# Performance work log

Hardware: AMD Instinct MI355X
Metric: run time of the kernel (lower is better)

The kernel has to match this reference:

```python
import jax, jax.numpy as jnp
import numpy as np
from jax import lax

RO = 4.0            # snake_config.ro (feature-map downsample ratio)
N_ADJ = 4           # snake_config.adj_num -> kernel = 2*4+1 = 9
K = 2 * N_ADJ + 1
DIL = (1, 1, 1, 2, 2, 4, 4)   # dilations of the 7 Snake residual circular convs
NMS_RADIUS = 2      # radius used in the iterative refinement cls_nms


def circ_conv(x, w, b, d):
    """Dilated circular conv along polygon axis. x:[N,C,P], w:[O,I,K]."""
    pad = N_ADJ * d
    xp = jnp.concatenate([x[..., -pad:], x, x[..., :pad]], axis=-1)
    y = lax.conv_general_dilated(xp, w, window_strides=(1,), padding='VALID',
                                 rhs_dilation=(d,),
                                 dimension_numbers=('NCH', 'OIH', 'NCH'))
    return y + b[None, :, None]


def conv1x1(x, w, b):
    # x:[N,C,P], w:[O,C] -> [N,O,P]
    return jnp.einsum('ncp,oc->nop', x, w) + b[None, :, None]


def bilinear_gather(cnn_feature, poly, ind):
    """grid_sample-style bilinear sampling (align_corners=False, zero pad).
    cnn_feature:[B,C,H,W], poly:[N,P,2] pixel coords, ind:[N] image index.
    Returns [N,C,P]."""
    B, C, H, W = cnn_feature.shape
    x = poly[..., 0] - 0.5
    y = poly[..., 1] - 0.5
    x0 = jnp.floor(x); y0 = jnp.floor(y)
    wx = x - x0; wy = y - y0
    x0i = x0.astype(jnp.int32); y0i = y0.astype(jnp.int32)

    def tap(yi, xi):
        valid = (xi >= 0) & (xi < W) & (yi >= 0) & (yi < H)
        xi_c = jnp.clip(xi, 0, W - 1)
        yi_c = jnp.clip(yi, 0, H - 1)
        f = cnn_feature[ind[:, None], :, yi_c, xi_c]  # [N,P,C]
        return f * valid[..., None]

    f00 = tap(y0i, x0i);     f01 = tap(y0i, x0i + 1)
    f10 = tap(y0i + 1, x0i); f11 = tap(y0i + 1, x0i + 1)
    out = (f00 * ((1 - wx) * (1 - wy))[..., None]
           + f01 * (wx * (1 - wy))[..., None]
           + f10 * ((1 - wx) * wy)[..., None]
           + f11 * (wx * wy)[..., None])
    return out.transpose(0, 2, 1)  # [N,C,P]


def cls_nms(cls, radius):
    """Circular local-max suppression of per-vertex scores. cls:[N,P,1]."""
    c = cls[..., 0]
    m = jnp.max(jnp.stack([jnp.roll(c, s, axis=1)
                           for s in range(-radius, radius + 1)], 0), axis=0)
    return jnp.where(c >= m, c, 0.0)[..., None]


def snake_body(x, head_w, head_b, res_w, res_b, fusion_w, fusion_b,
               pred1_w, pred1_b, pred2_w, pred2_b, pred3_w, pred3_b,
               cls1_w, cls1_b, cls2_w, cls2_b, cls3_w, cls3_b):
    h = jax.nn.relu(circ_conv(x, head_w, head_b, 1))
    states = [h]
    for i in range(7):  # fixed 7 residual layers, structurally distinct dilations
        r = jax.nn.relu(circ_conv(states[-1], res_w[i], res_b[i], DIL[i]))
        states.append(r + states[-1])
    state = jnp.concatenate(states, axis=1)                 # [N, 8*128, P]
    g = conv1x1(state, fusion_w, fusion_b)                  # [N, 256, P]
    g = jnp.max(g, axis=2, keepdims=True)
    g = jnp.broadcast_to(g, (state.shape[0], g.shape[1], state.shape[2]))
    state = jnp.concatenate([g, state], axis=1)             # [N, 1280, P]

    def head3(w1, b1, w2, b2, w3, b3):
        h1 = jax.nn.relu(conv1x1(state, w1, b1))
        h2 = jax.nn.relu(conv1x1(h1, w2, b2))
        return conv1x1(h2, w3, b3)

    offset = head3(pred1_w, pred1_b, pred2_w, pred2_b, pred3_w, pred3_b)  # [N,2,P]
    cls = head3(cls1_w, cls1_b, cls2_w, cls2_b, cls3_w, cls3_b)           # [N,1,P]
    return offset, cls


def setup_inputs() -> dict:
    key = jax.random.key(0)
    ks = jax.random.split(key, 32)
    B, C, H, W = 4, 64, 128, 128
    N, P = 512, 128
    SD = 128  # state_dim
    FD = 64 + 2 + 1  # feature_dim for iterative evolve_gcn
    std = 0.01  # conv init: normal(0, 0.01), bias 0 (matches module init)
    inp = {
        'cnn_feature': jax.random.normal(ks[0], (B, C, H, W), jnp.float32),
        'i_it_py': jax.random.uniform(ks[1], (N, P, 2), jnp.float32) * (W - 1),
        'c_it_py': jax.random.normal(ks[2], (N, P, 2), jnp.float32) * 0.2,
        'it_cls': jax.random.uniform(ks[3], (N, P), jnp.float32),
        'ind': jax.random.randint(ks[4], (N,), 0, B, jnp.int32),
        'head_w': jax.random.normal(ks[5], (SD, FD, K), jnp.float32) * std,
        'head_b': jnp.zeros((SD,), jnp.float32),
        'res_w': jax.random.normal(ks[6], (7, SD, SD, K), jnp.float32) * std,
        'res_b': jnp.zeros((7, SD), jnp.float32),
        'fusion_w': jax.random.normal(ks[7], (256, 8 * SD), jnp.float32) * std,
        'fusion_b': jnp.zeros((256,), jnp.float32),
        'pred1_w': jax.random.normal(ks[8], (256, 8 * SD + 256), jnp.float32) * std,
        'pred1_b': jnp.zeros((256,), jnp.float32),
        'pred2_w': jax.random.normal(ks[9], (64, 256), jnp.float32) * std,
        'pred2_b': jnp.zeros((64,), jnp.float32),
        'pred3_w': jax.random.normal(ks[10], (2, 64), jnp.float32) * std,
        'pred3_b': jnp.zeros((2,), jnp.float32),
        'cls1_w': jax.random.normal(ks[11], (256, 8 * SD + 256), jnp.float32) * std,
        'cls1_b': jnp.zeros((256,), jnp.float32),
        'cls2_w': jax.random.normal(ks[12], (64, 256), jnp.float32) * std,
        'cls2_b': jnp.zeros((64,), jnp.float32),
        'cls3_w': jax.random.normal(ks[13], (1, 64), jnp.float32) * std,
        'cls3_b': jnp.zeros((1,), jnp.float32),
    }
    return inp


def reference(cnn_feature, i_it_py, c_it_py, it_cls, ind,
              head_w, head_b, res_w, res_b, fusion_w, fusion_b,
              pred1_w, pred1_b, pred2_w, pred2_b, pred3_w, pred3_b,
              cls1_w, cls1_b, cls2_w, cls2_b, cls3_w, cls3_b):
    # evolve_poly: gather CNN features at vertices, concat scaled canonical
    # coords + per-vertex cls, run Snake, add offsets, NMS sigmoid scores.
    feat = bilinear_gather(cnn_feature, i_it_py, ind)        # [N,64,P]
    c = (c_it_py * RO).transpose(0, 2, 1)                    # [N,2,P]
    x = jnp.concatenate([feat, c, it_cls[:, None, :]], axis=1)  # [N,67,P]
    offset, cls = snake_body(x, head_w, head_b, res_w, res_b, fusion_w, fusion_b,
                             pred1_w, pred1_b, pred2_w, pred2_b, pred3_w, pred3_b,
                             cls1_w, cls1_b, cls2_w, cls2_b, cls3_w, cls3_b)
    i_poly = i_it_py * RO + offset.transpose(0, 2, 1)        # [N,P,2]
    cls = cls.transpose(0, 2, 1)                             # [N,P,1]
    nms = cls_nms(jax.nn.sigmoid(cls), NMS_RADIUS)           # [N,P,1]
    return i_poly, cls, nms
```

## Files before the change

### kernel.cpp

```cpp
#include <hip/hip_runtime.h>
#include <math.h>

typedef __attribute__((ext_vector_type(8))) short bf16x8;
typedef __attribute__((ext_vector_type(4))) float f32x4;

#define UOFF_CAW 0L
#define UOFF_FAW 2359296L
#define UOFF_H1W 2883584L
#define UOFF_W2F 3932160L
#define NB_TOT   3997696L
#define OFF_W1G  1998848L
#define OFF_DYN  2129920L
#define REPACK_N 4128768L

__device__ inline ushort f2bf_rne(float x) {
  uint u = __float_as_uint(x);
  return (ushort)((u + 0x7FFFu + ((u >> 16) & 1u)) >> 16);
}
__device__ inline void split_bf(float x, ushort& h, ushort& l) {
  uint u = __float_as_uint(x);
  uint hb = (u + 0x7FFFu + ((u >> 16) & 1u)) & 0xFFFF0000u;
  h = (ushort)(hb >> 16);
  l = f2bf_rne(x - __uint_as_float(hb));
}
__device__ inline ushort bfsel(float w, int split) {
  uint u = __float_as_uint(w);
  uint hb = (u + 0x7FFFu + ((u >> 16) & 1u)) & 0xFFFF0000u;
  if (split == 0) return (ushort)(hb >> 16);
  float lo = w - __uint_as_float(hb);
  uint ul = __float_as_uint(lo);
  return (ushort)((ul + 0x7FFFu + ((ul >> 16) & 1u)) >> 16);
}
__device__ inline bf16x8 asb(uint4 a) {
  union { uint4 u; bf16x8 v; } x; x.u = a; return x.v;
}
__device__ inline f32x4 MFMA_(bf16x8 a, bf16x8 b, f32x4 c) {
  return __builtin_amdgcn_mfma_f32_16x16x32_bf16(a, b, c, 0, 0, 0);
}
__device__ inline void bar_lgkm() {
  asm volatile("s_waitcnt lgkmcnt(0)" ::: "memory");
  __builtin_amdgcn_s_barrier();
}

__device__ inline void read_frag_pair(const char* xb, int pc, int g, int ic,
                                      bf16x8& bh, bf16x8& bl) {
  const int s0 = (pc & 7) << 4;
  const char* a = xb + pc * 512 + (((ic * 64 + (g << 4))) ^ s0);
  bh = asb(*(const uint4*)a);
  bl = asb(*(const uint4*)(a + 256));
}

__global__ void k_repack(const float* __restrict__ head_w, const float* __restrict__ res_w,
                         const float* __restrict__ fusion_w,
                         const float* __restrict__ pred1_w, const float* __restrict__ cls1_w,
                         const float* __restrict__ pred2_w, const float* __restrict__ cls2_w,
                         float* __restrict__ ws) {
  const long j = (long)blockIdx.x * 256 + threadIdx.x;
  if (j >= REPACK_N) return;
  if (j < NB_TOT) {
    ushort* wsu = (ushort*)ws;
    float w;
    if (j < UOFF_FAW) {
      int e = (int)(j & 7); long q = j >> 3;
      int lane = (int)(q & 63); q >>= 6;
      int mt = (int)(q & 1); q >>= 1;
      int split = (int)(q & 1); q >>= 1;
      int ic = (int)(q & 3); q >>= 2;
      int tap = (int)(q % 9); q /= 9;
      int mp = (int)(q & 3); int l = (int)(q >> 2);
      int gg = lane >> 4;
      int kl = (e < 4) ? (4 * gg + e) : (16 + 4 * gg + e - 4);
      int m = mp * 32 + mt * 16 + (lane & 15);
      int i = ic * 32 + kl;
      if (l == 0) w = (i < 67) ? head_w[((long)m * 67 + i) * 9 + tap] : 0.f;
      else        w = res_w[(((long)(l - 1) * 128 + m) * 128 + i) * 9 + tap];
      wsu[j] = bfsel(w, split);
    } else if (j < UOFF_H1W) {
      long jj = j - UOFF_FAW;
      int e = (int)(jj & 7); long q = jj >> 3;
      int lane = (int)(q & 63); q >>= 6;
      int mt = (int)(q & 1); q >>= 1;
      int split = (int)(q & 1); q >>= 1;
      int ic = (int)(q & 3); q >>= 2;
      int fm2 = (int)(q & 7); int l = (int)(q >> 3);
      int gg = lane >> 4;
      int kl = (e < 4) ? (4 * gg + e) : (16 + 4 * gg + e - 4);
      int m = fm2 * 32 + mt * 16 + (lane & 15);
      int i = ic * 32 + kl;
      w = fusion_w[(long)m * 1024 + l * 128 + i];
      wsu[j] = bfsel(w, split);
    } else if (j < UOFF_W2F) {
      long jj = j - UOFF_H1W;
      int e = (int)(jj & 7); long q = jj >> 3;
      int lane = (int)(q & 63); q >>= 6;
      int mt = (int)(q & 1); q >>= 1;
      int split = (int)(q & 1); q >>= 1;
      int ic = (int)(q & 3); q >>= 2;
      int slab = (int)(q & 7); q >>= 3;
      int mp = (int)(q & 7); int blk = (int)(q >> 3);
      int gg = lane >> 4;
      int kl = (e < 4) ? (4 * gg + e) : (16 + 4 * gg + e - 4);
      int m = blk * 256 + mp * 32 + mt * 16 + (lane & 15);
      int k = slab * 128 + ic * 32 + kl;
      w = (m < 256) ? pred1_w[(long)m * 1280 + 256 + k] : cls1_w[(long)(m - 256) * 1280 + 256 + k];
      wsu[j] = bfsel(w, split);
    } else {
      long jj = j - UOFF_W2F;
      int e = (int)(jj & 7); long q = jj >> 3;
      int lane = (int)(q & 63); q >>= 6;
      int split = (int)(q & 1); q >>= 1;
      int ic = (int)(q & 7); q >>= 3;
      int mfr = (int)(q & 3); int blk = (int)(q >> 2);
      int gg = lane >> 4;
      int kl = (e < 4) ? (4 * gg + e) : (16 + 4 * gg + e - 4);
      int m = mfr * 16 + (lane & 15);
      int k = ic * 32 + kl;
      w = blk ? cls2_w[(long)m * 256 + k] : pred2_w[(long)m * 256 + k];
      wsu[j] = bfsel(w, split);
    }
  } else {
    long q = j - NB_TOT; int o = (int)(q & 511); int c = (int)(q >> 9);
    ws[OFF_W1G + q] = (o < 256) ? pred1_w[(long)o * 1280 + c] : cls1_w[(long)(o - 256) * 1280 + c];
  }
}

__global__ __launch_bounds__(1024) __attribute__((amdgpu_waves_per_eu(4)))
void k_fused(const float* __restrict__ cnn, const float* __restrict__ i_it,
             const float* __restrict__ c_it, const float* __restrict__ cls_in,
             const int* __restrict__ ind,
             const ushort* __restrict__ CAW, const ushort* __restrict__ FAW,
             const ushort* __restrict__ H1W, const ushort* __restrict__ W2F,
             const float* __restrict__ head_b, const float* __restrict__ res_b,
             const float* __restrict__ fus_b, const float* __restrict__ W1G,
             const float* __restrict__ p1b, const float* __restrict__ c1b,
             const float* __restrict__ p2b, const float* __restrict__ c2b,
             const float* __restrict__ p3w, const float* __restrict__ p3b,
             const float* __restrict__ c3w, const float* __restrict__ c3b,
             float* __restrict__ states, float* __restrict__ out, int p0) {
  __shared__ uint4 xt4[4096];
  __shared__ float scr[512];
  __shared__ float sg[256];
  __shared__ float hg_s[512];
  char* xb = (char*)xt4;
  const int ln = blockIdx.x, n = p0 + ln, t = threadIdx.x;
  const int lane = t & 63, li = lane & 15, g = lane >> 4;
  const int wv = __builtin_amdgcn_readfirstlane(t >> 6);
  const int mp = wv & 3, np = wv >> 2;
  const int fm2 = wv & 7, fq = wv >> 3;
  const int mw = wv & 7, qw = wv >> 3;

  {
    const int p = t & 127, qg = t >> 7;
    const long nb = (long)n * 128 + p;
    const int sw = p & 7;
    if (qg < 4) {
      const float gx = i_it[nb * 2 + 0] - 0.5f;
      const float gy = i_it[nb * 2 + 1] - 0.5f;
      const float fx = floorf(gx), fy = floorf(gy);
      const float wx = gx - fx, wy = gy - fy;
      const int x0 = (int)fx, y0 = (int)fy, x1 = x0 + 1, y1 = y0 + 1;
      const bool vx0 = (x0 >= 0) & (x0 < 128), vx1 = (x1 >= 0) & (x1 < 128);
      const bool vy0 = (y0 >= 0) & (y0 < 128), vy1 = (y1 >= 0) & (y1 < 128);
      const int x0c = min(max(x0, 0), 127), x1c = min(max(x1, 0), 127);
      const int y0c = min(max(y0, 0), 127), y1c = min(max(y1, 0), 127);
      const float w00 = (vx0 && vy0) ? (1.f - wx) * (1.f - wy) : 0.f;
      const float w01 = (vx1 && vy0) ? wx * (1.f - wy) : 0.f;
      const float w10 = (vx0 && vy1) ? (1.f - wx) * wy : 0.f;
      const float w11 = (vx1 && vy1) ? wx * wy : 0.f;
      const long base = (long)ind[n] * (64L * 16384);
      const int a00 = y0c * 128 + x0c, a01 = y0c * 128 + x1c;
      const int a10 = y1c * 128 + x0c, a11 = y1c * 128 + x1c;
#pragma unroll
      for (int qq = 0; qq < 4; qq++) {
        ushort hh[4], ll[4];
#pragma unroll
        for (int cc = 0; cc < 4; cc++) {
          const int c = qg * 16 + qq * 4 + cc;
          const float* f = cnn + base + (long)c * 16384;
          float x = f[a00] * w00 + f[a01] * w01 + f[a10] * w10 + f[a11] * w11;
          split_bf(x, hh[cc], ll[cc]);
        }
        const int G = ((qg >> 1) * 4 + qq) ^ sw;
        char* a = xb + p * 512 + G * 16 + (qg & 1) * 8;
        *(uint2*)a = make_uint2((uint)hh[0] | ((uint)hh[1] << 16), (uint)hh[2] | ((uint)hh[3] << 16));
        *(uint2*)(a + 256) = make_uint2((uint)ll[0] | ((uint)ll[1] << 16), (uint)ll[2] | ((uint)ll[3] << 16));
      }
    } else {
#pragma unroll
      for (int qq = 0; qq < 4; qq++) {
        ushort hh[4], ll[4];
        if (qg == 4 && qq == 0) {
          float v0 = c_it[nb * 2 + 0] * 4.f, v1 = c_it[nb * 2 + 1] * 4.f, v2 = cls_in[nb];
          split_bf(v0, hh[0], ll[0]); split_bf(v1, hh[1], ll[1]); split_bf(v2, hh[2], ll[2]);
          hh[3] = 0; ll[3] = 0;
        } else {
          hh[0] = hh[1] = hh[2] = hh[3] = 0; ll[0] = ll[1] = ll[2] = ll[3] = 0;
        }
        const int G = ((qg >> 1) * 4 + qq) ^ sw;
        char* a = xb + p * 512 + G * 16 + (qg & 1) * 8;
        *(uint2*)a = make_uint2((uint)hh[0] | ((uint)hh[1] << 16), (uint)hh[2] | ((uint)hh[3] << 16));
        *(uint2*)(a + 256) = make_uint2((uint)ll[0] | ((uint)ll[1] << 16), (uint)ll[2] | ((uint)ll[3] << 16));
      }
    }
  }
  __syncthreads();

  const f32x4 fz = {0.f, 0.f, 0.f, 0.f};
  f32x4 facc[2][4];
#pragma unroll
  for (int a = 0; a < 2; a++)
#pragma unroll
    for (int b = 0; b < 4; b++) facc[a][b] = fz;

  const uint4* caw = (const uint4*)CAW;
  const uint4* faw = (const uint4*)FAW;
  uint4* stq = (uint4*)(states + (long)ln * 114688);

  for (int l = 0; l < 8; l++) {
    const int dil = (l >= 6) ? 4 : ((l >= 4) ? 2 : 1);
    const int nic = (l == 0) ? 3 : 4;
    if (l > 0) {
      uint4* dst = stq + (long)(l - 1) * 4096;
#pragma unroll
      for (int k = 0; k < 4; k++) dst[k * 1024 + t] = xt4[k * 1024 + t];
      const uint4* fawl = faw + ((long)((l - 1) * 8 + fm2)) * 1024 + lane;
#pragma unroll
      for (int ic = 0; ic < 4; ic++) {
        const uint4* w0 = fawl + ic * 256;
        const bf16x8 Ah0 = asb(w0[0]),   Ah1 = asb(w0[64]);
        const bf16x8 Al0 = asb(w0[128]), Al1 = asb(w0[192]);
#pragma unroll
        for (int nt = 0; nt < 4; nt++) {
          const int pc = fq * 64 + nt * 16 + li;
          bf16x8 bh, bl;
          read_frag_pair(xb, pc, g, ic, bh, bl);
          facc[0][nt] = MFMA_(Ah0, bh, facc[0][nt]);
          facc[1][nt] = MFMA_(Ah1, bh, facc[1][nt]);
          facc[0][nt] = MFMA_(Ah0, bl, facc[0][nt]);
          facc[1][nt] = MFMA_(Ah1, bl, facc[1][nt]);
          facc[0][nt] = MFMA_(Al0, bh, facc[0][nt]);
          facc[1][nt] = MFMA_(Al1, bh, facc[1][nt]);
        }
      }
    }
    f32x4 cacc[2][2];
    cacc[0][0] = fz; cacc[0][1] = fz; cacc[1][0] = fz; cacc[1][1] = fz;
    const uint4* cawl = caw + ((long)(l * 4 + mp)) * 9216;
    for (int tap = 0; tap < 9; tap++) {
      const int shift = (tap - 4) * dil;
      const int pc0 = (np * 32 + li + shift + 128) & 127;
      const int pc1 = (np * 32 + 16 + li + shift + 128) & 127;
      const uint4* cawt = cawl + tap * 1024 + lane;
      for (int ic = 0; ic < nic; ic++) {
        bf16x8 bh0, bl0, bh1, bl1;
        read_frag_pair(xb, pc0, g, ic, bh0, bl0);
        read_frag_pair(xb, pc1, g, ic, bh1, bl1);
        const uint4* w0 = cawt + ic * 256;
        const bf16x8 Ah0 = asb(w0[0]),   Ah1 = asb(w0[64]);
        const bf16x8 Al0 = asb(w0[128]), Al1 = asb(w0[192]);
        cacc[0][0] = MFMA_(Ah0, bh0, cacc[0][0]);
        cacc[0][1] = MFMA_(Ah0, bh1, cacc[0][1]);
        cacc[1][0] = MFMA_(Ah1, bh0, cacc[1][0]);
        cacc[1][1] = MFMA_(Ah1, bh1, cacc[1][1]);
        cacc[0][0] = MFMA_(Ah0, bl0, cacc[0][0]);
        cacc[0][1] = MFMA_(Ah0, bl1, cacc[0][1]);
        cacc[1][0] = MFMA_(Ah1, bl0, cacc[1][0]);
        cacc[1][1] = MFMA_(Ah1, bl1, cacc[1][1]);
        cacc[0][0] = MFMA_(Al0, bh0, cacc[0][0]);
        cacc[0][1] = MFMA_(Al0, bh1, cacc[0][1]);
        cacc[1][0] = MFMA_(Al1, bh0, cacc[1][0]);
        cacc[1][1] = MFMA_(Al1, bh1, cacc[1][1]);
      }
    }
    bar_lgkm();
    {
      const float* bsrc = (l == 0) ? head_b : (res_b + (l - 1) * 128);
      const float4 b0 = *(const float4*)&bsrc[mp * 32 + g * 4];
      const float4 b1 = *(const float4*)&bsrc[mp * 32 + 16 + g * 4];
#pragma unroll
      for (int nt = 0; nt < 2; nt++) {
        const int p = np * 32 + nt * 16 + li;
        const int X = (mp * 64 + g * 16) ^ ((p & 7) << 4);
        char* a = xb + p * 512 + X;
        float v[8];
        v[0] = fmaxf(cacc[0][nt][0] + b0.x, 0.f);
        v[1] = fmaxf(cacc[0][nt][1] + b0.y, 0.f);
        v[2] = fmaxf(cacc[0][nt][2] + b0.z, 0.f);
        v[3] = fmaxf(cacc[0][nt][3] + b0.w, 0.f);
        v[4] = fmaxf(cacc[1][nt][0] + b1.x, 0.f);
        v[5] = fmaxf(cacc[1][nt][1] + b1.y, 0.f);
        v[6] = fmaxf(cacc[1][nt][2] + b1.z, 0.f);
        v[7] = fmaxf(cacc[1][nt][3] + b1.w, 0.f);
        if (l > 0) {
          const uint4 oh = *(const uint4*)a;
          const uint4 ol = *(const uint4*)(a + 256);
          const uint hw[4] = {oh.x, oh.y, oh.z, oh.w};
          const uint lw[4] = {ol.x, ol.y, ol.z, ol.w};
#pragma unroll
          for (int k = 0; k < 8; k++) {
            const uint hh = (k & 1) ? (hw[k >> 1] & 0xFFFF0000u) : ((hw[k >> 1] & 0xFFFFu) << 16);
            const uint ll = (k & 1) ? (lw[k >> 1] & 0xFFFF0000u) : ((lw[k >> 1] & 0xFFFFu) << 16);
            v[k] += __uint_as_float(hh) + __uint_as_float(ll);
          }
        }
        ushort hh[8], ll[8];
#pragma unroll
        for (int k = 0; k < 8; k++) split_bf(v[k], hh[k], ll[k]);
        *(uint4*)a = make_uint4((uint)hh[0] | ((uint)hh[1] << 16), (uint)hh[2] | ((uint)hh[3] << 16),
                                (uint)hh[4] | ((uint)hh[5] << 16), (uint)hh[6] | ((uint)hh[7] << 16));
        *(uint4*)(a + 256) = make_uint4((uint)ll[0] | ((uint)ll[1] << 16), (uint)ll[2] | ((uint)ll[3] << 16),
                                        (uint)ll[4] | ((uint)ll[5] << 16), (uint)ll[6] | ((uint)ll[7] << 16));
      }
    }
    __syncthreads();
  }

  {
    const uint4* fawl = faw + ((long)(7 * 8 + fm2)) * 1024 + lane;
#pragma unroll
    for (int ic = 0; ic < 4; ic++) {
      const uint4* w0 = fawl + ic * 256;
      const bf16x8 Ah0 = asb(w0[0]),   Ah1 = asb(w0[64]);
      const bf16x8 Al0 = asb(w0[128]), Al1 = asb(w0[192]);
#pragma unroll
      for (int nt = 0; nt < 4; nt++) {
        const int pc = fq * 64 + nt * 16 + li;
        bf16x8 bh, bl;
        read_frag_pair(xb, pc, g, ic, bh, bl);
        facc[0][nt] = MFMA_(Ah0, bh, facc[0][nt]);
        facc[1][nt] = MFMA_(Ah1, bh, facc[1][nt]);
        facc[0][nt] = MFMA_(Ah0, bl, facc[0][nt]);
        facc[1][nt] = MFMA_(Ah1, bl, facc[1][nt]);
        facc[0][nt] = MFMA_(Al0, bh, facc[0][nt]);
        facc[1][nt] = MFMA_(Al1, bh, facc[1][nt]);
      }
    }
  }

#pragma unroll
  for (int mt = 0; mt < 2; mt++) {
#pragma unroll
    for (int r = 0; r < 4; r++) {
      float m = fmaxf(fmaxf(facc[mt][0][r], facc[mt][1][r]),
                      fmaxf(facc[mt][2][r], facc[mt][3][r]));
#pragma unroll
      for (int s = 1; s < 16; s <<= 1) m = fmaxf(m, __shfl_xor(m, s, 64));
      if (li == 0) scr[(fm2 * 32 + mt * 16 + g * 4 + r) * 2 + fq] = m;
    }
  }
  asm volatile("s_waitcnt vmcnt(0)" ::: "memory");
  bar_lgkm();
  if (t < 256) sg[t] = fmaxf(scr[2 * t], scr[2 * t + 1]) + fus_b[t];

  const uint4* sp = (const uint4*)stq;
  uint4 stg[4];
#pragma unroll
  for (int k = 0; k < 4; k++) stg[k] = sp[k * 1024 + t];
  bar_lgkm();

  if (t < 512) {
    float s = (t < 256) ? p1b[t] : c1b[t - 256];
    const float* w = W1G + t;
#pragma unroll 8
    for (int c = 0; c < 256; c++) s = fmaf(w[(long)c * 512], sg[c], s);
    hg_s[t] = s;
  }

  const uint4* aw = (const uint4*)H1W;
  f32x4 hacc[4][4];
#pragma unroll
  for (int f = 0; f < 4; f++)
#pragma unroll
    for (int c = 0; c < 4; c++) hacc[f][c] = fz;

#pragma unroll
  for (int ic = 0; ic < 4; ic++) {
    const uint4* w00 = aw + ((long)((2 * mw + 0) * 8 + 7)) * 1024 + ic * 256 + lane;
    const uint4* w01 = aw + ((long)((2 * mw + 1) * 8 + 7)) * 1024 + ic * 256 + lane;
    const bf16x8 Ah0 = asb(w00[0]),   Ah1 = asb(w00[64]);
    const bf16x8 Al0 = asb(w00[128]), Al1 = asb(w00[192]);
    const bf16x8 Ah2 = asb(w01[0]),   Ah3 = asb(w01[64]);
    const bf16x8 Al2 = asb(w01[128]), Al3 = asb(w01[192]);
#pragma unroll
    for (int nt = 0; nt < 4; nt++) {
      const int pc = qw * 64 + nt * 16 + li;
      bf16x8 bh, bl;
      read_frag_pair(xb, pc, g, ic, bh, bl);
      hacc[0][nt] = MFMA_(Ah0, bh, hacc[0][nt]);
      hacc[1][nt] = MFMA_(Ah1, bh, hacc[1][nt]);
      hacc[2][nt] = MFMA_(Ah2, bh, hacc[2][nt]);
      hacc[3][nt] = MFMA_(Ah3, bh, hacc[3][nt]);
      hacc[0][nt] = MFMA_(Ah0, bl, hacc[0][nt]);
      hacc[1][nt] = MFMA_(Ah1, bl, hacc[1][nt]);
      hacc[2][nt] = MFMA_(Ah2, bl, hacc[2][nt]);
      hacc[3][nt] = MFMA_(Ah3, bl, hacc[3][nt]);
      hacc[0][nt] = MFMA_(Al0, bh, hacc[0][nt]);
      hacc[1][nt] = MFMA_(Al1, bh, hacc[1][nt]);
      hacc[2][nt] = MFMA_(Al2, bh, hacc[2][nt]);
      hacc[3][nt] = MFMA_(Al3, bh, hacc[3][nt]);
    }
  }
  for (int s = 0; s < 7; s++) {
    bar_lgkm();
#pragma unroll
    for (int k = 0; k < 4; k++) xt4[k * 1024 + t] = stg[k];
    bar_lgkm();
    if (s < 6) {
#pragma unroll
      for (int k = 0; k < 4; k++) stg[k] = sp[(long)(s + 1) * 4096 + k * 1024 + t];
    }
#pragma unroll
    for (int ic = 0; ic < 4; ic++) {
      const uint4* w00 = aw + ((long)((2 * mw + 0) * 8 + s)) * 1024 + ic * 256 + lane;
      const uint4* w01 = aw + ((long)((2 * mw + 1) * 8 + s)) * 1024 + ic * 256 + lane;
      const bf16x8 Ah0 = asb(w00[0]),   Ah1 = asb(w00[64]);
      const bf16x8 Al0 = asb(w00[128]), Al1 = asb(w00[192]);
      const bf16x8 Ah2 = asb(w01[0]),   Ah3 = asb(w01[64]);
      const bf16x8 Al2 = asb(w01[128]), Al3 = asb(w01[192]);
#pragma unroll
      for (int nt = 0; nt < 4; nt++) {
        const int pc = qw * 64 + nt * 16 + li;
        bf16x8 bh, bl;
        read_frag_pair(xb, pc, g, ic, bh, bl);
        hacc[0][nt] = MFMA_(Ah0, bh, hacc[0][nt]);
        hacc[1][nt] = MFMA_(Ah1, bh, hacc[1][nt]);
        hacc[2][nt] = MFMA_(Ah2, bh, hacc[2][nt]);
        hacc[3][nt] = MFMA_(Ah3, bh, hacc[3][nt]);
        hacc[0][nt] = MFMA_(Ah0, bl, hacc[0][nt]);
        hacc[1][nt] = MFMA_(Ah1, bl, hacc[1][nt]);
        hacc[2][nt] = MFMA_(Ah2, bl, hacc[2][nt]);
        hacc[3][nt] = MFMA_(Ah3, bl, hacc[3][nt]);
        hacc[0][nt] = MFMA_(Al0, bh, hacc[0][nt]);
        hacc[1][nt] = MFMA_(Al1, bh, hacc[1][nt]);
        hacc[2][nt] = MFMA_(Al2, bh, hacc[2][nt]);
        hacc[3][nt] = MFMA_(Al3, bh, hacc[3][nt]);
      }
    }
  }
  bar_lgkm();

#pragma unroll
  for (int f = 0; f < 4; f++) {
    const float4 hq = *(const float4*)&hg_s[mw * 64 + f * 16 + g * 4];
#pragma unroll
    for (int nt = 0; nt < 4; nt++) {
      hacc[f][nt][0] = fmaxf(hacc[f][nt][0] + hq.x, 0.f);
      hacc[f][nt][1] = fmaxf(hacc[f][nt][1] + hq.y, 0.f);
      hacc[f][nt][2] = fmaxf(hacc[f][nt][2] + hq.z, 0.f);
      hacc[f][nt][3] = fmaxf(hacc[f][nt][3] + hq.w, 0.f);
    }
  }

  const uint4* w2 = (const uint4*)W2F;
  f32x4 a2q[4];
  for (int q = 0; q < 4; q++) {
    a2q[q] = fz;
    if (qw == (q >> 1)) {
#pragma unroll
      for (int fp = 0; fp < 4; fp += 2) {
        const int kc = 2 * mw + (fp >> 1);
#pragma unroll
        for (int ntl = 0; ntl < 2; ntl++) {
          const int nt = 2 * (q & 1) + ntl;
          const int pl = ntl * 16 + li;
          char* a = xb + pl * 2048 + ((kc * 64 + g * 16) ^ ((pl & 7) << 4));
          ushort hh[8], ll[8];
#pragma unroll
          for (int e = 0; e < 4; e++) { split_bf(hacc[fp][nt][e], hh[e], ll[e]); }
#pragma unroll
          for (int e = 0; e < 4; e++) { split_bf(hacc[fp + 1][nt][e], hh[4 + e], ll[4 + e]); }
          *(uint4*)a = make_uint4((uint)hh[0] | ((uint)hh[1] << 16), (uint)hh[2] | ((uint)hh[3] << 16),
                                  (uint)hh[4] | ((uint)hh[5] << 16), (uint)hh[6] | ((uint)hh[7] << 16));
          *(uint4*)(a + 1024) = make_uint4((uint)ll[0] | ((uint)ll[1] << 16), (uint)ll[2] | ((uint)ll[3] << 16),
                                           (uint)ll[4] | ((uint)ll[5] << 16), (uint)ll[6] | ((uint)ll[7] << 16));
        }
      }
    }
    bar_lgkm();
    {
      const int blkc = mw >> 2;
      const int pl = qw * 16 + li;
#pragma unroll
      for (int ic8 = 0; ic8 < 8; ic8++) {
        const int kc = blkc * 8 + ic8;
        const uint4* wb = w2 + (((long)(blkc * 4 + (mw & 3)) * 8 + ic8) * 2) * 64 + lane;
        const bf16x8 Ah = asb(wb[0]), Al = asb(wb[64]);
        const char* ba = xb + pl * 2048 + ((kc * 64 + g * 16) ^ ((pl & 7) << 4));
        const bf16x8 bh = asb(*(const uint4*)ba);
        const bf16x8 bl = asb(*(const uint4*)(ba + 1024));
        a2q[q] = MFMA_(Ah, bh, a2q[q]);
        a2q[q] = MFMA_(Ah, bl, a2q[q]);
        a2q[q] = MFMA_(Al, bh, a2q[q]);
      }
    }
    bar_lgkm();
  }

  {
    float* h2L = (float*)xb;
#pragma unroll
    for (int q = 0; q < 4; q++) {
#pragma unroll
      for (int e = 0; e < 4; e++) {
        const int row = mw * 16 + g * 4 + e;
        const float bb = (mw < 4) ? p2b[row] : c2b[row - 64];
        h2L[row * 128 + q * 32 + qw * 16 + li] = fmaxf(a2q[q][e] + bb, 0.f);
      }
    }
  }
  bar_lgkm();

  {
    const float* h2L = (const float*)xb;
    float sig = 0.f;
    const int pp = t & 127;
    if (t < 128) {
      float o0v = p3b[0], o1v = p3b[1], cv = c3b[0];
      for (int j = 0; j < 64; j++) {
        const float hp = h2L[j * 128 + pp];
        const float hc = h2L[(64 + j) * 128 + pp];
        o0v = fmaf(p3w[j], hp, o0v);
        o1v = fmaf(p3w[64 + j], hp, o1v);
        cv = fmaf(c3w[j], hc, cv);
      }
      const long ip = ((long)n * 128 + pp) * 2;
      out[ip + 0] = i_it[ip + 0] * 4.f + o0v;
      out[ip + 1] = i_it[ip + 1] * 4.f + o1v;
      out[131072 + (long)n * 128 + pp] = cv;
      sig = 1.f / (1.f + expf(-cv));
      scr[pp] = sig;
    }
    bar_lgkm();
    if (t < 128) {
      float m = scr[pp];
#pragma unroll
      for (int s = 1; s <= 2; s++) {
        m = fmaxf(m, scr[(pp + s) & 127]);
        m = fmaxf(m, scr[(pp + 128 - s) & 127]);
      }
      out[196608 + (long)n * 128 + pp] = (sig >= m) ? sig : 0.f;
    }
  }
}

extern "C" void kernel_launch(void* const* d_in, const int* in_sizes, int n_in,
                              void* d_out, int out_size, void* d_ws, size_t ws_size,
                              hipStream_t stream) {
  const float* cnn      = (const float*)d_in[0];
  const float* i_it     = (const float*)d_in[1];
  const float* c_it     = (const float*)d_in[2];
  const float* it_cls   = (const float*)d_in[3];
  const int*   ind      = (const int*)d_in[4];
  const float* head_w   = (const float*)d_in[5];
  const float* head_b   = (const float*)d_in[6];
  const float* res_w    = (const float*)d_in[7];
  const float* res_b    = (const float*)d_in[8];
  const float* fusion_w = (const float*)d_in[9];
  const float* fusion_b = (const float*)d_in[10];
  const float* pred1_w  = (const float*)d_in[11];
  const float* pred1_b  = (const float*)d_in[12];
  const float* pred2_w  = (const float*)d_in[13];
  const float* pred2_b  = (const float*)d_in[14];
  const float* pred3_w  = (const float*)d_in[15];
  const float* pred3_b  = (const float*)d_in[16];
  const float* cls1_w   = (const float*)d_in[17];
  const float* cls1_b   = (const float*)d_in[18];
  const float* cls2_w   = (const float*)d_in[19];
  const float* cls2_b   = (const float*)d_in[20];
  const float* cls3_w   = (const float*)d_in[21];
  const float* cls3_b   = (const float*)d_in[22];
  float* ws = (float*)d_ws;
  float* out = (float*)d_out;
  const ushort* wsu = (const ushort*)d_ws;

  k_repack<<<(int)((REPACK_N + 255) / 256), 256, 0, stream>>>(
      head_w, res_w, fusion_w, pred1_w, cls1_w, pred2_w, cls2_w, ws);

  long avail_f = (long)(ws_size / 4) - OFF_DYN;
  long Cl = avail_f / 114688;
  int C = (Cl >= 512) ? 512 : ((Cl >= 256) ? 256 : (int)(Cl < 1 ? 1 : Cl));
  float* states = ws + OFF_DYN;

  for (int p0 = 0; p0 < 512; p0 += C) {
    int Cc = (512 - p0 < C) ? (512 - p0) : C;
    k_fused<<<Cc, 1024, 0, stream>>>(cnn, i_it, c_it, it_cls, ind,
                                     wsu + UOFF_CAW, wsu + UOFF_FAW,
                                     wsu + UOFF_H1W, wsu + UOFF_W2F,
                                     head_b, res_b, fusion_b, ws + OFF_W1G,
                                     pred1_b, cls1_b, pred2_b, cls2_b,
                                     pred3_w, pred3_b, cls3_w, cls3_b,
                                     states, out, p0);
  }
}
```

Baseline: 1.033 ms.

## Fuse fusion and pred1/cls1 projections into per-layer accumulation, drop state spill

Concatenates the fusion conv weights and the state part of pred1/cls1 into one 768-row weight matrix, so each layer's state is multiplied into all three accumulations right after it is produced. This removes the global-memory spill and reload of the eight 128x128 layer states and the second pass over them. It also removes the chunked multi-launch loop in favour of a single launch. The cost is 24 accumulator tiles per wave instead of 8, which raises register pressure and may cut occupancy. The circular-conv inner loop is also reordered to load one B fragment pair at a time.

Measured after the change: 1.368 ms. +32.4%, slower.

```diff
diff --git a/kernel.cpp b/kernel.cpp
--- a/kernel.cpp
+++ b/kernel.cpp
@@ -5,12 +5,10 @@
 typedef __attribute__((ext_vector_type(4))) float f32x4;
 
 #define UOFF_CAW 0L
-#define UOFF_FAW 2359296L
-#define UOFF_H1W 2883584L
+#define UOFF_GW  2359296L
 #define UOFF_W2F 3932160L
 #define NB_TOT   3997696L
 #define OFF_W1G  1998848L
-#define OFF_DYN  2129920L
 #define REPACK_N 4128768L
 
 __device__ inline ushort f2bf_rne(float x) {
@@ -60,7 +58,7 @@
   if (j < NB_TOT) {
     ushort* wsu = (ushort*)ws;
     float w;
-    if (j < UOFF_FAW) {
+    if (j < UOFF_GW) {
       int e = (int)(j & 7); long q = j >> 3;
       int lane = (int)(q & 63); q >>= 6;
       int mt = (int)(q & 1); q >>= 1;
@@ -75,34 +73,21 @@
       if (l == 0) w = (i < 67) ? head_w[((long)m * 67 + i) * 9 + tap] : 0.f;
       else        w = res_w[(((long)(l - 1) * 128 + m) * 128 + i) * 9 + tap];
       wsu[j] = bfsel(w, split);
-    } else if (j < UOFF_H1W) {
-      long jj = j - UOFF_FAW;
+    } else if (j < UOFF_W2F) {
+      long jj = j - UOFF_GW;
       int e = (int)(jj & 7); long q = jj >> 3;
       int lane = (int)(q & 63); q >>= 6;
-      int mt = (int)(q & 1); q >>= 1;
       int split = (int)(q & 1); q >>= 1;
       int ic = (int)(q & 3); q >>= 2;
-      int fm2 = (int)(q & 7); int l = (int)(q >> 3);
+      int f = (int)(q % 3); q /= 3;
+      int wv = (int)(q & 15); int l = (int)(q >> 4);
       int gg = lane >> 4;
       int kl = (e < 4) ? (4 * gg + e) : (16 + 4 * gg + e - 4);
-      int m = fm2 * 32 + mt * 16 + (lane & 15);
-      int i = ic * 32 + kl;
-      w = fusion_w[(long)m * 1024 + l * 128 + i];
-      wsu[j] = bfsel(w, split);
-    } else if (j < UOFF_W2F) {
-      long jj = j - UOFF_H1W;
-      int e = (int)(jj & 7); long q = jj >> 3;
-      int lane = (int)(q & 63); q >>= 6;
-      int mt = (int)(q & 1); q >>= 1;
-      int split = (int)(q & 1); q >>= 1;
-      int ic = (int)(q & 3); q >>= 2;
-      int slab = (int)(q & 7); q >>= 3;
-      int mp = (int)(q & 7); int blk = (int)(q >> 3);
-      int gg = lane >> 4;
-      int kl = (e < 4) ? (4 * gg + e) : (16 + 4 * gg + e - 4);
-      int m = blk * 256 + mp * 32 + mt * 16 + (lane & 15);
-      int k = slab * 128 + ic * 32 + kl;
-      w = (m < 256) ? pred1_w[(long)m * 1280 + 256 + k] : cls1_w[(long)(m - 256) * 1280 + 256 + k];
+      int grow = wv * 48 + f * 16 + (lane & 15);
+      int k = ic * 32 + kl;
+      if (grow < 256)      w = fusion_w[(long)grow * 1024 + l * 128 + k];
+      else if (grow < 512) w = pred1_w[(long)(grow - 256) * 1280 + 256 + l * 128 + k];
+      else                 w = cls1_w[(long)(grow - 512) * 1280 + 256 + l * 128 + k];
       wsu[j] = bfsel(w, split);
     } else {
       long jj = j - UOFF_W2F;
@@ -128,25 +113,24 @@
 void k_fused(const float* __restrict__ cnn, const float* __restrict__ i_it,
              const float* __restrict__ c_it, const float* __restrict__ cls_in,
              const int* __restrict__ ind,
-             const ushort* __restrict__ CAW, const ushort* __restrict__ FAW,
-             const ushort* __restrict__ H1W, const ushort* __restrict__ W2F,
+             const ushort* __restrict__ CAW, const ushort* __restrict__ GW,
+             const ushort* __restrict__ W2F,
              const float* __restrict__ head_b, const float* __restrict__ res_b,
              const float* __restrict__ fus_b, const float* __restrict__ W1G,
              const float* __restrict__ p1b, const float* __restrict__ c1b,
              const float* __restrict__ p2b, const float* __restrict__ c2b,
              const float* __restrict__ p3w, const float* __restrict__ p3b,
              const float* __restrict__ c3w, const float* __restrict__ c3b,
-             float* __restrict__ states, float* __restrict__ out, int p0) {
+             float* __restrict__ out) {
   __shared__ uint4 xt4[4096];
-  __shared__ float scr[512];
+  __shared__ float scr[256];
   __shared__ float sg[256];
   __shared__ float hg_s[512];
   char* xb = (char*)xt4;
-  const int ln = blockIdx.x, n = p0 + ln, t = threadIdx.x;
+  const int n = blockIdx.x, t = threadIdx.x;
   const int lane = t & 63, li = lane & 15, g = lane >> 4;
   const int wv = __builtin_amdgcn_readfirstlane(t >> 6);
   const int mp = wv & 3, np = wv >> 2;
-  const int fm2 = wv & 7, fq = wv >> 3;
   const int mw = wv & 7, qw = wv >> 3;
 
   {
@@ -206,40 +190,42 @@
   __syncthreads();
 
   const f32x4 fz = {0.f, 0.f, 0.f, 0.f};
-  f32x4 facc[2][4];
-#pragma unroll
-  for (int a = 0; a < 2; a++)
-#pragma unroll
-    for (int b = 0; b < 4; b++) facc[a][b] = fz;
+  f32x4 acc[3][8];
+#pragma unroll
+  for (int f = 0; f < 3; f++)
+#pragma unroll
+    for (int c = 0; c < 8; c++) acc[f][c] = fz;
 
   const uint4* caw = (const uint4*)CAW;
-  const uint4* faw = (const uint4*)FAW;
-  uint4* stq = (uint4*)(states + (long)ln * 114688);
+  const uint4* gaw = (const uint4*)GW;
 
   for (int l = 0; l < 8; l++) {
     const int dil = (l >= 6) ? 4 : ((l >= 4) ? 2 : 1);
     const int nic = (l == 0) ? 3 : 4;
     if (l > 0) {
-      uint4* dst = stq + (long)(l - 1) * 4096;
-#pragma unroll
-      for (int k = 0; k < 4; k++) dst[k * 1024 + t] = xt4[k * 1024 + t];
-      const uint4* fawl = faw + ((long)((l - 1) * 8 + fm2)) * 1024 + lane;
+      const uint4* gwl = gaw + ((long)((l - 1) * 16 + wv)) * 1536 + lane;
 #pragma unroll
       for (int ic = 0; ic < 4; ic++) {
-        const uint4* w0 = fawl + ic * 256;
-        const bf16x8 Ah0 = asb(w0[0]),   Ah1 = asb(w0[64]);
-        const bf16x8 Al0 = asb(w0[128]), Al1 = asb(w0[192]);
-#pragma unroll
-        for (int nt = 0; nt < 4; nt++) {
-          const int pc = fq * 64 + nt * 16 + li;
+        const uint4* w0 = gwl + (0 * 4 + ic) * 128;
+        const uint4* w1 = gwl + (1 * 4 + ic) * 128;
+        const uint4* w2p = gwl + (2 * 4 + ic) * 128;
+        const bf16x8 Ah0 = asb(w0[0]), Al0 = asb(w0[64]);
+        const bf16x8 Ah1 = asb(w1[0]), Al1 = asb(w1[64]);
+        const bf16x8 Ah2 = asb(w2p[0]), Al2 = asb(w2p[64]);
+#pragma unroll
+        for (int nt = 0; nt < 8; nt++) {
+          const int pc = nt * 16 + li;
           bf16x8 bh, bl;
           read_frag_pair(xb, pc, g, ic, bh, bl);
-          facc[0][nt] = MFMA_(Ah0, bh, facc[0][nt]);
-          facc[1][nt] = MFMA_(Ah1, bh, facc[1][nt]);
-          facc[0][nt] = MFMA_(Ah0, bl, facc[0][nt]);
-          facc[1][nt] = MFMA_(Ah1, bl, facc[1][nt]);
-          facc[0][nt] = MFMA_(Al0, bh, facc[0][nt]);
-          facc[1][nt] = MFMA_(Al1, bh, facc[1][nt]);
+          acc[0][nt] = MFMA_(Ah0, bh, acc[0][nt]);
+          acc[1][nt] = MFMA_(Ah1, bh, acc[1][nt]);
+          acc[2][nt] = MFMA_(Ah2, bh, acc[2][nt]);
+          acc[0][nt] = MFMA_(Ah0, bl, acc[0][nt]);
+          acc[1][nt] = MFMA_(Ah1, bl, acc[1][nt]);
+          acc[2][nt] = MFMA_(Ah2, bl, acc[2][nt]);
+          acc[0][nt] = MFMA_(Al0, bh, acc[0][nt]);
+          acc[1][nt] = MFMA_(Al1, bh, acc[1][nt]);
+          acc[2][nt] = MFMA_(Al2, bh, acc[2][nt]);
         }
       }
     }
@@ -252,24 +238,24 @@
       const int pc1 = (np * 32 + 16 + li + shift + 128) & 127;
       const uint4* cawt = cawl + tap * 1024 + lane;
       for (int ic = 0; ic < nic; ic++) {
-        bf16x8 bh0, bl0, bh1, bl1;
-        read_frag_pair(xb, pc0, g, ic, bh0, bl0);
-        read_frag_pair(xb, pc1, g, ic, bh1, bl1);
         const uint4* w0 = cawt + ic * 256;
         const bf16x8 Ah0 = asb(w0[0]),   Ah1 = asb(w0[64]);
         const bf16x8 Al0 = asb(w0[128]), Al1 = asb(w0[192]);
-        cacc[0][0] = MFMA_(Ah0, bh0, cacc[0][0]);
-        cacc[0][1] = MFMA_(Ah0, bh1, cacc[0][1]);
-        cacc[1][0] = MFMA_(Ah1, bh0, cacc[1][0]);
-        cacc[1][1] = MFMA_(Ah1, bh1, cacc[1][1]);
-        cacc[0][0] = MFMA_(Ah0, bl0, cacc[0][0]);
-        cacc[0][1] = MFMA_(Ah0, bl1, cacc[0][1]);
-        cacc[1][0] = MFMA_(Ah1, bl0, cacc[1][0]);
-        cacc[1][1] = MFMA_(Ah1, bl1, cacc[1][1]);
-        cacc[0][0] = MFMA_(Al0, bh0, cacc[0][0]);
-        cacc[0][1] = MFMA_(Al0, bh1, cacc[0][1]);
-        cacc[1][0] = MFMA_(Al1, bh0, cacc[1][0]);
-        cacc[1][1] = MFMA_(Al1, bh1, cacc[1][1]);
+        bf16x8 bh, bl;
+        read_frag_pair(xb, pc0, g, ic, bh, bl);
+        cacc[0][0] = MFMA_(Ah0, bh, cacc[0][0]);
+        cacc[1][0] = MFMA_(Ah1, bh, cacc[1][0]);
+        cacc[0][0] = MFMA_(Ah0, bl, cacc[0][0]);
+        cacc[1][0] = MFMA_(Ah1, bl, cacc[1][0]);
+        cacc[0][0] = MFMA_(Al0, bh, cacc[0][0]);
+        cacc[1][0] = MFMA_(Al1, bh, cacc[1][0]);
+        read_frag_pair(xb, pc1, g, ic, bh, bl);
+        cacc[0][1] = MFMA_(Ah0, bh, cacc[0][1]);
+        cacc[1][1] = MFMA_(Ah1, bh, cacc[1][1]);
+        cacc[0][1] = MFMA_(Ah0, bl, cacc[0][1]);
+        cacc[1][1] = MFMA_(Ah1, bl, cacc[1][1]);
+        cacc[0][1] = MFMA_(Al0, bh, cacc[0][1]);
+        cacc[1][1] = MFMA_(Al1, bh, cacc[1][1]);
       }
     }
     bar_lgkm();
@@ -316,46 +302,50 @@
   }
 
   {
-    const uint4* fawl = faw + ((long)(7 * 8 + fm2)) * 1024 + lane;
+    const uint4* gwl = gaw + ((long)(7 * 16 + wv)) * 1536 + lane;
 #pragma unroll
     for (int ic = 0; ic < 4; ic++) {
-      const uint4* w0 = fawl + ic * 256;
-      const bf16x8 Ah0 = asb(w0[0]),   Ah1 = asb(w0[64]);
-      const bf16x8 Al0 = asb(w0[128]), Al1 = asb(w0[192]);
-#pragma unroll
-      for (int nt = 0; nt < 4; nt++) {
-        const int pc = fq * 64 + nt * 16 + li;
+      const uint4* w0 = gwl + (0 * 4 + ic) * 128;
+      const uint4* w1 = gwl + (1 * 4 + ic) * 128;
+      const uint4* w2p = gwl + (2 * 4 + ic) * 128;
+      const bf16x8 Ah0 = asb(w0[0]), Al0 = asb(w0[64]);
+      const bf16x8 Ah1 = asb(w1[0]), Al1 = asb(w1[64]);
+      const bf16x8 Ah2 = asb(w2p[0]), Al2 = asb(w2p[64]);
+#pragma unroll
+      for (int nt = 0; nt < 8; nt++) {
+        const int pc = nt * 16 + li;
         bf16x8 bh, bl;
         read_frag_pair(xb, pc, g, ic, bh, bl);
-        facc[0][nt] = MFMA_(Ah0, bh, facc[0][nt]);
-        facc[1][nt] = MFMA_(Ah1, bh, facc[1][nt]);
-        facc[0][nt] = MFMA_(Ah0, bl, facc[0][nt]);
-        facc[1][nt] = MFMA_(Ah1, bl, facc[1][nt]);
-        facc[0][nt] = MFMA_(Al0, bh, facc[0][nt]);
-        facc[1][nt] = MFMA_(Al1, bh, facc[1][nt]);
-      }
-    }
-  }
-
-#pragma unroll
-  for (int mt = 0; mt < 2; mt++) {
-#pragma unroll
-    for (int r = 0; r < 4; r++) {
-      float m = fmaxf(fmaxf(facc[mt][0][r], facc[mt][1][r]),
-                      fmaxf(facc[mt][2][r], facc[mt][3][r]));
-#pragma unroll
-      for (int s = 1; s < 16; s <<= 1) m = fmaxf(m, __shfl_xor(m, s, 64));
-      if (li == 0) scr[(fm2 * 32 + mt * 16 + g * 4 + r) * 2 + fq] = m;
-    }
-  }
-  asm volatile("s_waitcnt vmcnt(0)" ::: "memory");
+        acc[0][nt] = MFMA_(Ah0, bh, acc[0][nt]);
+        acc[1][nt] = MFMA_(Ah1, bh, acc[1][nt]);
+        acc[2][nt] = MFMA_(Ah2, bh, acc[2][nt]);
+        acc[0][nt] = MFMA_(Ah0, bl, acc[0][nt]);
+        acc[1][nt] = MFMA_(Ah1, bl, acc[1][nt]);
+        acc[2][nt] = MFMA_(Ah2, bl, acc[2][nt]);
+        acc[0][nt] = MFMA_(Al0, bh, acc[0][nt]);
+        acc[1][nt] = MFMA_(Al1, bh, acc[1][nt]);
+        acc[2][nt] = MFMA_(Al2, bh, acc[2][nt]);
+      }
+    }
+  }
+
+#pragma unroll
+  for (int f = 0; f < 3; f++) {
+    const int base = wv * 48 + f * 16;
+    if (base < 256) {
+#pragma unroll
+      for (int e = 0; e < 4; e++) {
+        float m = acc[f][0][e];
+#pragma unroll
+        for (int nt = 1; nt < 8; nt++) m = fmaxf(m, acc[f][nt][e]);
+#pragma unroll
+        for (int s = 1; s < 16; s <<= 1) m = fmaxf(m, __shfl_xor(m, s, 64));
+        if (li == 0) scr[base + g * 4 + e] = m;
+      }
+    }
+  }
   bar_lgkm();
-  if (t < 256) sg[t] = fmaxf(scr[2 * t], scr[2 * t + 1]) + fus_b[t];
-
-  const uint4* sp = (const uint4*)stq;
-  uint4 stg[4];
-#pragma unroll
-  for (int k = 0; k < 4; k++) stg[k] = sp[k * 1024 + t];
+  if (t < 256) sg[t] = scr[t] + fus_b[t];
   bar_lgkm();
 
   if (t < 512) {
@@ -365,89 +355,20 @@
     for (int c = 0; c < 256; c++) s = fmaf(w[(long)c * 512], sg[c], s);
     hg_s[t] = s;
   }
-
-  const uint4* aw = (const uint4*)H1W;
-  f32x4 hacc[4][4];
-#pragma unroll
-  for (int f = 0; f < 4; f++)
-#pragma unroll
-    for (int c = 0; c < 4; c++) hacc[f][c] = fz;
-
-#pragma unroll
-  for (int ic = 0; ic < 4; ic++) {
-    const uint4* w00 = aw + ((long)((2 * mw + 0) * 8 + 7)) * 1024 + ic * 256 + lane;
-    const uint4* w01 = aw + ((long)((2 * mw + 1) * 8 + 7)) * 1024 + ic * 256 + lane;
-    const bf16x8 Ah0 = asb(w00[0]),   Ah1 = asb(w00[64]);
-    const bf16x8 Al0 = asb(w00[128]), Al1 = asb(w00[192]);
-    const bf16x8 Ah2 = asb(w01[0]),   Ah3 = asb(w01[64]);
-    const bf16x8 Al2 = asb(w01[128]), Al3 = asb(w01[192]);
-#pragma unroll
-    for (int nt = 0; nt < 4; nt++) {
-      const int pc = qw * 64 + nt * 16 + li;
-      bf16x8 bh, bl;
-      read_frag_pair(xb, pc, g, ic, bh, bl);
-      hacc[0][nt] = MFMA_(Ah0, bh, hacc[0][nt]);
-      hacc[1][nt] = MFMA_(Ah1, bh, hacc[1][nt]);
-      hacc[2][nt] = MFMA_(Ah2, bh, hacc[2][nt]);
-      hacc[3][nt] = MFMA_(Ah3, bh, hacc[3][nt]);
-      hacc[0][nt] = MFMA_(Ah0, bl, hacc[0][nt]);
-      hacc[1][nt] = MFMA_(Ah1, bl, hacc[1][nt]);
-      hacc[2][nt] = MFMA_(Ah2, bl, hacc[2][nt]);
-      hacc[3][nt] = MFMA_(Ah3, bl, hacc[3][nt]);
-      hacc[0][nt] = MFMA_(Al0, bh, hacc[0][nt]);
-      hacc[1][nt] = MFMA_(Al1, bh, hacc[1][nt]);
-      hacc[2][nt] = MFMA_(Al2, bh, hacc[2][nt]);
-      hacc[3][nt] = MFMA_(Al3, bh, hacc[3][nt]);
-    }
-  }
-  for (int s = 0; s < 7; s++) {
-    bar_lgkm();
-#pragma unroll
-    for (int k = 0; k < 4; k++) xt4[k * 1024 + t] = stg[k];
-    bar_lgkm();
-    if (s < 6) {
-#pragma unroll
-      for (int k = 0; k < 4; k++) stg[k] = sp[(long)(s + 1) * 4096 + k * 1024 + t];
-    }
-#pragma unroll
-    for (int ic = 0; ic < 4; ic++) {
-      const uint4* w00 = aw + ((long)((2 * mw + 0) * 8 + s)) * 1024 + ic * 256 + lane;
-      const uint4* w01 = aw + ((long)((2 * mw + 1) * 8 + s)) * 1024 + ic * 256 + lane;
-      const bf16x8 Ah0 = asb(w00[0]),   Ah1 = asb(w00[64]);
-      const bf16x8 Al0 = asb(w00[128]), Al1 = asb(w00[192]);
-      const bf16x8 Ah2 = asb(w01[0]),   Ah3 = asb(w01[64]);
-      const bf16x8 Al2 = asb(w01[128]), Al3 = asb(w01[192]);
-#pragma unroll
-      for (int nt = 0; nt < 4; nt++) {
-        const int pc = qw * 64 + nt * 16 + li;
-        bf16x8 bh, bl;
-        read_frag_pair(xb, pc, g, ic, bh, bl);
-        hacc[0][nt] = MFMA_(Ah0, bh, hacc[0][nt]);
-        hacc[1][nt] = MFMA_(Ah1, bh, hacc[1][nt]);
-        hacc[2][nt] = MFMA_(Ah2, bh, hacc[2][nt]);
-        hacc[3][nt] = MFMA_(Ah3, bh, hacc[3][nt]);
-        hacc[0][nt] = MFMA_(Ah0, bl, hacc[0][nt]);
-        hacc[1][nt] = MFMA_(Ah1, bl, hacc[1][nt]);
-        hacc[2][nt] = MFMA_(Ah2, bl, hacc[2][nt]);
-        hacc[3][nt] = MFMA_(Ah3, bl, hacc[3][nt]);
-        hacc[0][nt] = MFMA_(Al0, bh, hacc[0][nt]);
-        hacc[1][nt] = MFMA_(Al1, bh, hacc[1][nt]);
-        hacc[2][nt] = MFMA_(Al2, bh, hacc[2][nt]);
-        hacc[3][nt] = MFMA_(Al3, bh, hacc[3][nt]);
-      }
-    }
-  }
   bar_lgkm();
 
 #pragma unroll
-  for (int f = 0; f < 4; f++) {
-    const float4 hq = *(const float4*)&hg_s[mw * 64 + f * 16 + g * 4];
-#pragma unroll
-    for (int nt = 0; nt < 4; nt++) {
-      hacc[f][nt][0] = fmaxf(hacc[f][nt][0] + hq.x, 0.f);
-      hacc[f][nt][1] = fmaxf(hacc[f][nt][1] + hq.y, 0.f);
-      hacc[f][nt][2] = fmaxf(hacc[f][nt][2] + hq.z, 0.f);
-      hacc[f][nt][3] = fmaxf(hacc[f][nt][3] + hq.w, 0.f);
+  for (int f = 0; f < 3; f++) {
+    const int base = wv * 48 + f * 16;
+    if (base >= 256) {
+      const float4 hq = *(const float4*)&hg_s[base - 256 + g * 4];
+#pragma unroll
+      for (int nt = 0; nt < 8; nt++) {
+        acc[f][nt][0] = fmaxf(acc[f][nt][0] + hq.x, 0.f);
+        acc[f][nt][1] = fmaxf(acc[f][nt][1] + hq.y, 0.f);
+        acc[f][nt][2] = fmaxf(acc[f][nt][2] + hq.z, 0.f);
+        acc[f][nt][3] = fmaxf(acc[f][nt][3] + hq.w, 0.f);
+      }
     }
   }
 
@@ -455,24 +376,27 @@
   f32x4 a2q[4];
   for (int q = 0; q < 4; q++) {
     a2q[q] = fz;
-    if (qw == (q >> 1)) {
-#pragma unroll
-      for (int fp = 0; fp < 4; fp += 2) {
-        const int kc = 2 * mw + (fp >> 1);
+#pragma unroll
+    for (int f = 0; f < 3; f++) {
+      const int base = wv * 48 + f * 16;
+      if (base >= 256) {
+        const int r1b = base - 256 + g * 4;
+        const int kc = r1b >> 5;
+        const int kic = r1b & 31;
+        const int gp = (kic & 15) >> 2;
+        const int half = kic >> 4;
 #pragma unroll
         for (int ntl = 0; ntl < 2; ntl++) {
-          const int nt = 2 * (q & 1) + ntl;
+          const int nt = 2 * q + ntl;
           const int pl = ntl * 16 + li;
-          char* a = xb + pl * 2048 + ((kc * 64 + g * 16) ^ ((pl & 7) << 4));
-          ushort hh[8], ll[8];
-#pragma unroll
-          for (int e = 0; e < 4; e++) { split_bf(hacc[fp][nt][e], hh[e], ll[e]); }
-#pragma unroll
-          for (int e = 0; e < 4; e++) { split_bf(hacc[fp + 1][nt][e], hh[4 + e], ll[4 + e]); }
-          *(uint4*)a = make_uint4((uint)hh[0] | ((uint)hh[1] << 16), (uint)hh[2] | ((uint)hh[3] << 16),
-                                  (uint)hh[4] | ((uint)hh[5] << 16), (uint)hh[6] | ((uint)hh[7] << 16));
-          *(uint4*)(a + 1024) = make_uint4((uint)ll[0] | ((uint)ll[1] << 16), (uint)ll[2] | ((uint)ll[3] << 16),
-                                           (uint)ll[4] | ((uint)ll[5] << 16), (uint)ll[6] | ((uint)ll[7] << 16));
+          char* a = xb + pl * 2048 + ((kc * 64 + gp * 16) ^ ((pl & 7) << 4)) + half * 8;
+          ushort hh[4], ll[4];
+          split_bf(acc[f][nt][0], hh[0], ll[0]);
+          split_bf(acc[f][nt][1], hh[1], ll[1]);
+          split_bf(acc[f][nt][2], hh[2], ll[2]);
+          split_bf(acc[f][nt][3], hh[3], ll[3]);
+          *(uint2*)a = make_uint2((uint)hh[0] | ((uint)hh[1] << 16), (uint)hh[2] | ((uint)hh[3] << 16));
+          *(uint2*)(a + 1024) = make_uint2((uint)ll[0] | ((uint)ll[1] << 16), (uint)ll[2] | ((uint)ll[3] << 16));
         }
       }
     }
@@ -576,19 +500,9 @@
   k_repack<<<(int)((REPACK_N + 255) / 256), 256, 0, stream>>>(
       head_w, res_w, fusion_w, pred1_w, cls1_w, pred2_w, cls2_w, ws);
 
-  long avail_f = (long)(ws_size / 4) - OFF_DYN;
-  long Cl = avail_f / 114688;
-  int C = (Cl >= 512) ? 512 : ((Cl >= 256) ? 256 : (int)(Cl < 1 ? 1 : Cl));
-  float* states = ws + OFF_DYN;
-
-  for (int p0 = 0; p0 < 512; p0 += C) {
-    int Cc = (512 - p0 < C) ? (512 - p0) : C;
-    k_fused<<<Cc, 1024, 0, stream>>>(cnn, i_it, c_it, it_cls, ind,
-                                     wsu + UOFF_CAW, wsu + UOFF_FAW,
-                                     wsu + UOFF_H1W, wsu + UOFF_W2F,
-                                     head_b, res_b, fusion_b, ws + OFF_W1G,
-                                     pred1_b, cls1_b, pred2_b, cls2_b,
-                                     pred3_w, pred3_b, cls3_w, cls3_b,
-                                     states, out, p0);
-  }
-}
+  k_fused<<<512, 1024, 0, stream>>>(cnn, i_it, c_it, it_cls, ind,
+                                    wsu + UOFF_CAW, wsu + UOFF_GW, wsu + UOFF_W2F,
+                                    head_b, res_b, fusion_b, ws + OFF_W1G,
+                                    pred1_b, cls1_b, pred2_b, cls2_b,
+                                    pred3_w, pred3_b, cls3_w, cls3_b, out);
+}
```
